# Kernel tuning notes

Measured on AMD Instinct MI355X. Metric: run time of the kernel, lower is better.

Reference implementation:

```python
import jax, jax.numpy as jnp
import numpy as np
import math

B, ENC, SEQ, H = 32, 512, 1024, 8
HD = SEQ // H  # 128
EPS = 1e-5


def setup_inputs() -> dict:
    key = jax.random.key(0)
    ks = jax.random.split(key, 7)
    s = 0.02
    return {
        "x": jax.random.normal(ks[0], (B, ENC, SEQ), jnp.float32),
        "ln_g": jnp.ones((SEQ,), jnp.float32),
        "ln_b": jnp.zeros((SEQ,), jnp.float32),
        "w_in": jax.random.normal(ks[1], (3 * SEQ, SEQ), jnp.float32) * s,
        "b_in": jnp.zeros((3 * SEQ,), jnp.float32),
        "w_m1a": jax.random.normal(ks[2], (HD, HD), jnp.float32) * s,
        "b_m1a": jnp.zeros((HD,), jnp.float32),
        "w_m1b": jax.random.normal(ks[3], (1, HD), jnp.float32) * s,
        "b_m1b": jnp.zeros((1,), jnp.float32),
        "w_m2": jax.random.normal(ks[4], (1, ENC), jnp.float32) * s,
        "b_m2": jnp.zeros((1,), jnp.float32),
        "w_out": jax.random.normal(ks[5], (SEQ, 2 * SEQ), jnp.float32) * s,
        "b_out": jnp.zeros((SEQ,), jnp.float32),
    }


def reference(x, ln_g, ln_b, w_in, b_in, w_m1a, b_m1a, w_m1b, b_m1b,
              w_m2, b_m2, w_out, b_out):
    Bsz, N, S = x.shape  # N == enc_in, S == seq_len == d_model
    hd = S // H
    scale = 1.0 / math.sqrt(hd * N)

    # LayerNorm over last dim
    mu = jnp.mean(x, axis=-1, keepdims=True)
    var = jnp.mean(jnp.square(x - mu), axis=-1, keepdims=True)
    xn = (x - mu) * jax.lax.rsqrt(var + EPS) * ln_g + ln_b

    qkv = xn @ w_in.T + b_in  # [B, N, 3S]
    q, k, v = jnp.split(qkv, 3, axis=-1)
    # torch .view(B, H, N, hd) on contiguous [B, N, S] is a raw reshape
    q = q.reshape(Bsz, H, N, hd)
    k = k.reshape(Bsz, H, N, hd)
    v = v.reshape(Bsz, H, N, hd)

    def mlp1(t):  # [B,H,N,hd] -> [B,H,N]
        h1 = jnp.maximum(jnp.einsum('bhnd,ed->bhne', t, w_m1a) + b_m1a, 0.0)
        return jnp.einsum('bhne,e->bhn', h1, w_m1b[0]) + b_m1b[0]

    def mlp2(t):  # [B,H,N,hd] -> [B,H,hd] (Linear over N then ReLU)
        return jnp.maximum(jnp.einsum('bhnd,n->bhd', t, w_m2[0]) + b_m2[0], 0.0)

    # rank-1 outer-product scores, broadcast-multiplied into v
    s_qk = mlp1(q)[..., None] * mlp2(k)[:, :, None, :] * scale  # [B,H,N,hd]
    v1 = (s_qk * v).reshape(Bsz, N, S)
    s_kq = mlp1(k)[..., None] * mlp2(q)[:, :, None, :] * scale
    v2 = (s_kq * v).reshape(Bsz, N, S)

    out = jnp.concatenate([v1, v2], axis=-1) @ w_out.T + b_out  # [B,N,S]
    return out + x  # dropout is identity at eval
```

## Files before the change

### kernel.cpp

```cpp
#include <hip/hip_runtime.h>
#include <cstdint>
#include <cstddef>

#define BSZ   32
#define ENCN  512
#define SEQL  1024
#define MROWS (BSZ*ENCN)
#define N1    (3*SEQL)
#define K1    SEQL
#define N2    SEQL
#define K2    (2*SEQL)

typedef __bf16 bf16;
typedef __bf16 bf16x8 __attribute__((ext_vector_type(8)));
typedef __bf16 bf16x4 __attribute__((ext_vector_type(4)));
typedef float  f32x4  __attribute__((ext_vector_type(4)));
typedef int    i32x4  __attribute__((ext_vector_type(4)));
typedef int    i32x8  __attribute__((ext_vector_type(8)));

__device__ __forceinline__ void gl_lds16(const void* g, void* l) {
  __builtin_amdgcn_global_load_lds(
      (const __attribute__((address_space(1))) void*)(uintptr_t)g,
      (__attribute__((address_space(3))) void*)(uintptr_t)(uint32_t)(uintptr_t)l,
      16, 0, 0);
}

__device__ __forceinline__ f32x4 mfma16(bf16x8 a, bf16x8 b, f32x4 c) {
  return __builtin_amdgcn_mfma_f32_16x16x32_bf16(a, b, c, 0, 0, 0);
}

__device__ __forceinline__ uint32_t pk4_fp8(float a, float b, float c, float d) {
  int v = __builtin_amdgcn_cvt_pk_fp8_f32(a, b, 0, false);
  v = __builtin_amdgcn_cvt_pk_fp8_f32(c, d, v, true);
  return (uint32_t)v;
}

__global__ __launch_bounds__(256) void cvt_w_kernel(const float* __restrict__ w_in,
                                                    const float* __restrict__ w_out,
                                                    const float* __restrict__ w1a,
                                                    uint8_t* __restrict__ wi8,
                                                    uint8_t* __restrict__ wo8,
                                                    bf16* __restrict__ w1ab) {
  int idx = blockIdx.x * 256 + threadIdx.x;
  const int NWIN4 = (N1 * K1) / 4;
  const int NOUT4 = (N2 * K2) / 4;
  if (idx < NWIN4) {
    float4 v = ((const float4*)w_in)[idx];
    ((uint32_t*)wi8)[idx] = pk4_fp8(v.x * 64.f, v.y * 64.f, v.z * 64.f, v.w * 64.f);
  } else if (idx < NWIN4 + NOUT4) {
    int j = idx - NWIN4;
    float4 v = ((const float4*)w_out)[j];
    ((uint32_t*)wo8)[j] = pk4_fp8(v.x * 64.f, v.y * 64.f, v.z * 64.f, v.w * 64.f);
  } else {
    int j = idx - NWIN4 - NOUT4;
    float4 v = ((const float4*)w1a)[j];
    bf16x4 o = { (bf16)v.x, (bf16)v.y, (bf16)v.z, (bf16)v.w };
    ((bf16x4*)w1ab)[j] = o;
  }
}

__global__ __launch_bounds__(256) void ln_kernel(const float* __restrict__ x,
                                                 const float* __restrict__ g,
                                                 const float* __restrict__ bt,
                                                 uint8_t* __restrict__ xn8) {
  int row = blockIdx.x;
  int t = threadIdx.x;
  const float4 v = ((const float4*)(x + (size_t)row * SEQL))[t];
  float s  = v.x + v.y + v.z + v.w;
  float ss = v.x*v.x + v.y*v.y + v.z*v.z + v.w*v.w;
  for (int off = 32; off; off >>= 1) {
    s  += __shfl_down(s,  off, 64);
    ss += __shfl_down(ss, off, 64);
  }
  __shared__ float red[8];
  int w = t >> 6, l = t & 63;
  if (l == 0) { red[w] = s; red[w + 4] = ss; }
  __syncthreads();
  float st  = red[0] + red[1] + red[2] + red[3];
  float sst = red[4] + red[5] + red[6] + red[7];
  float mu   = st * (1.0f / SEQL);
  float var  = sst * (1.0f / SEQL) - mu * mu;
  float rstd = rsqrtf(var + 1e-5f);
  float4 gv = ((const float4*)g)[t];
  float4 bv = ((const float4*)bt)[t];
  float y0 = (v.x - mu) * rstd * gv.x + bv.x;
  float y1 = (v.y - mu) * rstd * gv.y + bv.y;
  float y2 = (v.z - mu) * rstd * gv.z + bv.z;
  float y3 = (v.w - mu) * rstd * gv.w + bv.w;
  ((uint32_t*)(xn8 + (size_t)row * SEQL))[t] = pk4_fp8(y0, y1, y2, y3);
}

template <int MODE, int SA, int SB>
__global__ __launch_bounds__(256) void gemm_fp8(const uint8_t* __restrict__ A,
                                                const uint8_t* __restrict__ Bw,
                                                const float* __restrict__ bias,
                                                const float* __restrict__ resid,
                                                void* __restrict__ Cout,
                                                int M, int N, int K) {
  __shared__ uint8_t Als[128 * 128];
  __shared__ uint8_t Bls[128 * 128];
  const int tid = threadIdx.x;
  const int w = tid >> 6, l = tid & 63;
  const int wm = w & 1, wn = w >> 1;
  const int q = l >> 4, li = l & 15;
  const int m0 = blockIdx.x * 128;
  const int n0 = blockIdx.y * 128;

  const int srow = tid >> 3;
  const int scol = ((tid & 7) ^ (srow & 7)) << 4;

  const int c0 = ((2 * q)     ^ (li & 7)) << 4;
  const int c1 = ((2 * q + 1) ^ (li & 7)) << 4;

  f32x4 acc[4][4] = {};

  for (int k0 = 0; k0 < K; k0 += 128) {
#pragma unroll
    for (int is = 0; is < 4; is++) {
      gl_lds16(A  + (size_t)(m0 + is * 32 + srow) * K + k0 + scol,
               (char*)Als + is * 4096 + w * 1024);
      gl_lds16(Bw + (size_t)(n0 + is * 32 + srow) * K + k0 + scol,
               (char*)Bls + is * 4096 + w * 1024);
    }
    __syncthreads();
    i32x8 af[4], bfg[4];
#pragma unroll
    for (int i = 0; i < 4; i++) {
      int r = wm * 64 + i * 16 + li;
      i32x4 lo = *(const i32x4*)&Als[r * 128 + c0];
      i32x4 hi = *(const i32x4*)&Als[r * 128 + c1];
      af[i] = i32x8{lo[0], lo[1], lo[2], lo[3], hi[0], hi[1], hi[2], hi[3]};
    }
#pragma unroll
    for (int j = 0; j < 4; j++) {
      int r = wn * 64 + j * 16 + li;
      i32x4 lo = *(const i32x4*)&Bls[r * 128 + c0];
      i32x4 hi = *(const i32x4*)&Bls[r * 128 + c1];
      bfg[j] = i32x8{lo[0], lo[1], lo[2], lo[3], hi[0], hi[1], hi[2], hi[3]};
    }
#pragma unroll
    for (int i = 0; i < 4; i++)
#pragma unroll
      for (int j = 0; j < 4; j++)
        acc[i][j] = __builtin_amdgcn_mfma_scale_f32_16x16x128_f8f6f4(
            af[i], bfg[j], acc[i][j], 0 , 0 ,
            0, SA, 0, SB);
    __syncthreads();
  }

#pragma unroll
  for (int i = 0; i < 4; i++)
#pragma unroll
    for (int j = 0; j < 4; j++) {
      int col = n0 + wn * 64 + j * 16 + li;
      float bv = bias[col];
#pragma unroll
      for (int r = 0; r < 4; r++) {
        int row = m0 + wm * 64 + i * 16 + q * 4 + r;
        float v = acc[i][j][r] + bv;
        if (MODE == 0) {
          ((bf16*)Cout)[(size_t)row * N + col] = (bf16)v;
        } else {
          ((float*)Cout)[(size_t)row * N + col] = v + resid[(size_t)row * N + col];
        }
      }
    }
}

__global__ __launch_bounds__(256) void mlp12_kernel(const bf16* __restrict__ qkv,
                                                    const bf16* __restrict__ w1ab,
                                                    const float* __restrict__ b1a,
                                                    const float* __restrict__ w1b,
                                                    const float* __restrict__ b1b,
                                                    const float* __restrict__ w2,
                                                    float* __restrict__ A1q,
                                                    float* __restrict__ A1k,
                                                    float* __restrict__ A2p) {
  __shared__ float red1[2][128];
  __shared__ float redm[16][128];
  __shared__ float w2s[128];
  const int bid = blockIdx.x;
  const int T = bid >> 10;
  const int rem = bid & 1023;
  const int bh = rem >> 2, quarter = rem & 3;
  const int tid = threadIdx.x;
  const int w = tid >> 6, l = tid & 63;
  const int wm = w & 1, wn = w >> 1;
  const int q = l >> 4, li = l & 15;
  const int R0 = bh * 64 + quarter * 16;
  const bf16* rbase = qkv + (size_t)R0 * N1 + T * 1024;

  if (tid < 128) w2s[tid] = w2[quarter * 128 + tid];

  bf16x8 bfrag[4][4];
  float b1av[4], w1bv[4];
#pragma unroll
  for (int j = 0; j < 4; j++) {
    int n = wn * 64 + j * 16 + li;
#pragma unroll
    for (int kq = 0; kq < 4; kq++)
      bfrag[kq][j] = *(const bf16x8*)&w1ab[n * 128 + kq * 32 + q * 8];
    b1av[j] = b1a[n];
    w1bv[j] = w1b[n];
  }

  f32x4 acc[4][4] = {};
#pragma unroll
  for (int kq = 0; kq < 4; kq++) {
#pragma unroll
    for (int i = 0; i < 4; i++) {
      int lc = wm * 64 + i * 16 + li;
      bf16x8 af = *(const bf16x8*)(rbase + (size_t)(lc >> 3) * N1
                                   + (lc & 7) * 128 + kq * 32 + q * 8);
#pragma unroll
      for (int j = 0; j < 4; j++)
        acc[i][j] = mfma16(af, bfrag[kq][j], acc[i][j]);
    }
  }
#pragma unroll
  for (int i = 0; i < 4; i++)
#pragma unroll
    for (int r = 0; r < 4; r++) {
      float s = 0.f;
#pragma unroll
      for (int j = 0; j < 4; j++)
        s += fmaxf(acc[i][j][r] + b1av[j], 0.f) * w1bv[j];
      for (int off = 1; off < 16; off <<= 1) s += __shfl_xor(s, off, 64);
      if (li == 0) red1[wn][wm * 64 + i * 16 + q * 4 + r] = s;
    }
  __syncthreads();
  if (tid < 128) {
    float v = red1[0][tid] + red1[1][tid] + b1b[0];
    (T ? A1k : A1q)[bh * 512 + quarter * 128 + tid] = v;
  }

  const int rg = tid >> 4, dg = tid & 15;
  const bf16* arow = rbase + (size_t)rg * N1 + dg * 8;
  float a8[8] = {0, 0, 0, 0, 0, 0, 0, 0};
#pragma unroll
  for (int cc = 0; cc < 8; cc++) {
    bf16x8 v = *(const bf16x8*)(arow + cc * 128);
    float wgt = w2s[rg * 8 + cc];
#pragma unroll
    for (int e = 0; e < 8; e++) a8[e] += (float)v[e] * wgt;
  }
#pragma unroll
  for (int e = 0; e < 8; e++) redm[rg][dg * 8 + e] = a8[e];
  __syncthreads();
  if (tid < 128) {
    float s = 0.f;
#pragma unroll
    for (int rg2 = 0; rg2 < 16; rg2++) s += redm[rg2][tid];
    A2p[(((size_t)T * 256 + bh) * 4 + quarter) * 128 + tid] = s;
  }
}

__global__ __launch_bounds__(256) void a2c_kernel(const float* __restrict__ A2p,
                                                  const float* __restrict__ b2,
                                                  float* __restrict__ A2q,
                                                  float* __restrict__ A2k) {
  int idx = blockIdx.x * 256 + threadIdx.x;
  int t = idx >> 15, r = idx & 32767;
  int bh = r >> 7, d = r & 127;
  const float* p = A2p + ((size_t)t * 256 + bh) * 512 + d;
  float s = p[0] + p[128] + p[256] + p[384] + b2[0];
  (t ? A2k : A2q)[r] = fmaxf(s, 0.f);
}

__global__ __launch_bounds__(256) void scale_kernel(const bf16* __restrict__ qkv,
                                                    const float* __restrict__ A1q,
                                                    const float* __restrict__ A1k,
                                                    const float* __restrict__ A2q,
                                                    const float* __restrict__ A2k,
                                                    uint8_t* __restrict__ Y) {
  size_t idx = ((size_t)blockIdx.x * 256 + threadIdx.x) * 8;
  int b = (int)(idx >> 19);
  int f = (int)(idx & 524287);
  int chunk = f >> 7;
  float a1q = A1q[b * 4096 + chunk] * 64.f;
  float a1k = A1k[b * 4096 + chunk] * 64.f;
  int a2i = b * 1024 + ((f >> 16) << 7) + (f & 127);
  float4 k0 = *(const float4*)&A2k[a2i];
  float4 k1 = *(const float4*)&A2k[a2i + 4];
  float4 q0 = *(const float4*)&A2q[a2i];
  float4 q1 = *(const float4*)&A2q[a2i + 4];
  int row = b * 512 + (f >> 10);
  int col = f & 1023;
  bf16x8 v = *(const bf16x8*)&qkv[(size_t)row * N1 + 2048 + col];
  float kk[8] = { k0.x, k0.y, k0.z, k0.w, k1.x, k1.y, k1.z, k1.w };
  float qq[8] = { q0.x, q0.y, q0.z, q0.w, q1.x, q1.y, q1.z, q1.w };
  float y1[8], y2[8];
#pragma unroll
  for (int e = 0; e < 8; e++) {
    float vv = (float)v[e];
    y1[e] = a1q * kk[e] * vv;
    y2[e] = a1k * qq[e] * vv;
  }
  uint8_t* yr = Y + (size_t)row * K2;
  ((uint32_t*)(yr + col))[0] = pk4_fp8(y1[0], y1[1], y1[2], y1[3]);
  ((uint32_t*)(yr + col))[1] = pk4_fp8(y1[4], y1[5], y1[6], y1[7]);
  ((uint32_t*)(yr + 1024 + col))[0] = pk4_fp8(y2[0], y2[1], y2[2], y2[3]);
  ((uint32_t*)(yr + 1024 + col))[1] = pk4_fp8(y2[4], y2[5], y2[6], y2[7]);
}

extern "C" void kernel_launch(void* const* d_in, const int* in_sizes, int n_in,
                              void* d_out, int out_size, void* d_ws, size_t ws_size,
                              hipStream_t stream) {
  const float* x     = (const float*)d_in[0];
  const float* ln_g  = (const float*)d_in[1];
  const float* ln_b  = (const float*)d_in[2];
  const float* w_in  = (const float*)d_in[3];
  const float* b_in  = (const float*)d_in[4];
  const float* w1a   = (const float*)d_in[5];
  const float* b1a   = (const float*)d_in[6];
  const float* w1b   = (const float*)d_in[7];
  const float* b1b   = (const float*)d_in[8];
  const float* w2    = (const float*)d_in[9];
  const float* b2    = (const float*)d_in[10];
  const float* w_out = (const float*)d_in[11];
  const float* b_out = (const float*)d_in[12];
  float* out = (float*)d_out;
  char* ws = (char*)d_ws;

  uint8_t* xn8  = (uint8_t*)(ws);
  bf16*    qkv  = (bf16*)   (ws + 16777216);
  uint8_t* Y8   = (uint8_t*)(ws + 117440512);
  uint8_t* wi8  = (uint8_t*)(ws + 150994944);
  uint8_t* wo8  = (uint8_t*)(ws + 154140672);
  bf16*    w1ab = (bf16*)   (ws + 156237824);
  float*   A1q  = (float*)  (ws + 156270592);
  float*   A1k  = (float*)  (ws + 156794880);
  float*   A2p  = (float*)  (ws + 157319168);
  float*   A2q  = (float*)  (ws + 158367744);
  float*   A2k  = (float*)  (ws + 158498816);

  cvt_w_kernel<<<5136, 256, 0, stream>>>(w_in, w_out, w1a, wi8, wo8, w1ab);
  ln_kernel<<<MROWS, 256, 0, stream>>>(x, ln_g, ln_b, xn8);
  gemm_fp8<0, 127, 121><<<dim3(MROWS / 128, N1 / 128), 256, 0, stream>>>(
      xn8, wi8, b_in, nullptr, qkv, MROWS, N1, K1);
  mlp12_kernel<<<2048, 256, 0, stream>>>(qkv, w1ab, b1a, w1b, b1b, w2, A1q, A1k, A2p);
  a2c_kernel<<<256, 256, 0, stream>>>(A2p, b2, A2q, A2k);
  scale_kernel<<<8192, 256, 0, stream>>>(qkv, A1q, A1k, A2q, A2k, Y8);
  gemm_fp8<1, 113, 121><<<dim3(MROWS / 128, N2 / 128), 256, 0, stream>>>(
      Y8, wo8, b_out, x, out, MROWS, N2, K2);
}
```

Before: 324.0 us.

## Store QKV intermediate as scaled FP8 and run MLP1 with FP8 MFMA

The QKV GEMM epilogue now writes FP8 values scaled by 64 instead of bf16, halving the intermediate's size and the write and read traffic in the MLP and scale kernels. MLP1 switches to FP8 MFMA with FP8 weights, and the scale factors are folded into the downstream kernels. The workspace layout is compacted and Y8 reuses the LN buffer region. The risk is lower precision in q/k/v, which feeds the rank-1 score products.

```diff
diff --git a/kernel.cpp b/kernel.cpp
--- a/kernel.cpp
+++ b/kernel.cpp
@@ -1,4 +1,5 @@
 #include <hip/hip_runtime.h>
+#include <hip/hip_fp8.h>
 #include <cstdint>
 #include <cstddef>
 
@@ -12,8 +13,6 @@
 #define K2    (2*SEQL)
 
 typedef __bf16 bf16;
-typedef __bf16 bf16x8 __attribute__((ext_vector_type(8)));
-typedef __bf16 bf16x4 __attribute__((ext_vector_type(4)));
 typedef float  f32x4  __attribute__((ext_vector_type(4)));
 typedef int    i32x4  __attribute__((ext_vector_type(4)));
 typedef int    i32x8  __attribute__((ext_vector_type(8)));
@@ -25,14 +24,20 @@
       16, 0, 0);
 }
 
-__device__ __forceinline__ f32x4 mfma16(bf16x8 a, bf16x8 b, f32x4 c) {
-  return __builtin_amdgcn_mfma_f32_16x16x32_bf16(a, b, c, 0, 0, 0);
-}
-
 __device__ __forceinline__ uint32_t pk4_fp8(float a, float b, float c, float d) {
   int v = __builtin_amdgcn_cvt_pk_fp8_f32(a, b, 0, false);
   v = __builtin_amdgcn_cvt_pk_fp8_f32(c, d, v, true);
   return (uint32_t)v;
+}
+__device__ __forceinline__ uint8_t pk1_fp8(float a) {
+  return (uint8_t)(__builtin_amdgcn_cvt_pk_fp8_f32(a, a, 0, false) & 0xff);
+}
+__device__ __forceinline__ float fp8_to_f(uint32_t b) {
+  __hip_fp8_e4m3 t; t.__x = (__hip_fp8_storage_t)b; return (float)t;
+}
+
+__device__ __forceinline__ f32x4 mfma8(long a, long b, f32x4 c) {
+  return __builtin_amdgcn_mfma_f32_16x16x32_fp8_fp8(a, b, c, 0, 0, 0);
 }
 
 __global__ __launch_bounds__(256) void cvt_w_kernel(const float* __restrict__ w_in,
@@ -40,23 +45,22 @@
                                                     const float* __restrict__ w1a,
                                                     uint8_t* __restrict__ wi8,
                                                     uint8_t* __restrict__ wo8,
-                                                    bf16* __restrict__ w1ab) {
+                                                    uint8_t* __restrict__ w1a8) {
   int idx = blockIdx.x * 256 + threadIdx.x;
   const int NWIN4 = (N1 * K1) / 4;
   const int NOUT4 = (N2 * K2) / 4;
+  const float4* src;
+  uint32_t* dst;
+  int j;
   if (idx < NWIN4) {
-    float4 v = ((const float4*)w_in)[idx];
-    ((uint32_t*)wi8)[idx] = pk4_fp8(v.x * 64.f, v.y * 64.f, v.z * 64.f, v.w * 64.f);
+    src = (const float4*)w_in;  dst = (uint32_t*)wi8;  j = idx;
   } else if (idx < NWIN4 + NOUT4) {
-    int j = idx - NWIN4;
-    float4 v = ((const float4*)w_out)[j];
-    ((uint32_t*)wo8)[j] = pk4_fp8(v.x * 64.f, v.y * 64.f, v.z * 64.f, v.w * 64.f);
+    src = (const float4*)w_out; dst = (uint32_t*)wo8;  j = idx - NWIN4;
   } else {
-    int j = idx - NWIN4 - NOUT4;
-    float4 v = ((const float4*)w1a)[j];
-    bf16x4 o = { (bf16)v.x, (bf16)v.y, (bf16)v.z, (bf16)v.w };
-    ((bf16x4*)w1ab)[j] = o;
-  }
+    src = (const float4*)w1a;   dst = (uint32_t*)w1a8; j = idx - NWIN4 - NOUT4;
+  }
+  float4 v = src[j];
+  dst[j] = pk4_fp8(v.x * 64.f, v.y * 64.f, v.z * 64.f, v.w * 64.f);
 }
 
 __global__ __launch_bounds__(256) void ln_kernel(const float* __restrict__ x,
@@ -91,12 +95,12 @@
 }
 
 template <int MODE, int SA, int SB>
-__global__ __launch_bounds__(256) void gemm_fp8(const uint8_t* __restrict__ A,
-                                                const uint8_t* __restrict__ Bw,
-                                                const float* __restrict__ bias,
-                                                const float* __restrict__ resid,
-                                                void* __restrict__ Cout,
-                                                int M, int N, int K) {
+__device__ __forceinline__ void gemm_fp8_impl(const uint8_t* __restrict__ A,
+                                              const uint8_t* __restrict__ Bw,
+                                              const float* __restrict__ bias,
+                                              const float* __restrict__ resid,
+                                              void* __restrict__ Cout,
+                                              int M, int N, int K) {
   __shared__ uint8_t Als[128 * 128];
   __shared__ uint8_t Bls[128 * 128];
   const int tid = threadIdx.x;
@@ -159,7 +163,7 @@
         int row = m0 + wm * 64 + i * 16 + q * 4 + r;
         float v = acc[i][j][r] + bv;
         if (MODE == 0) {
-          ((bf16*)Cout)[(size_t)row * N + col] = (bf16)v;
+          ((uint8_t*)Cout)[(size_t)row * N + col] = pk1_fp8(v * 64.f);
         } else {
           ((float*)Cout)[(size_t)row * N + col] = v + resid[(size_t)row * N + col];
         }
@@ -167,8 +171,22 @@
     }
 }
 
-__global__ __launch_bounds__(256) void mlp12_kernel(const bf16* __restrict__ qkv,
-                                                    const bf16* __restrict__ w1ab,
+__global__ __launch_bounds__(256) void gemm_qkv(const uint8_t* __restrict__ A,
+                                                const uint8_t* __restrict__ Bw,
+                                                const float* __restrict__ bias,
+                                                uint8_t* __restrict__ Cout) {
+  gemm_fp8_impl<0, 127, 121>(A, Bw, bias, nullptr, Cout, MROWS, N1, K1);
+}
+__global__ __launch_bounds__(256) void gemm_out(const uint8_t* __restrict__ A,
+                                                const uint8_t* __restrict__ Bw,
+                                                const float* __restrict__ bias,
+                                                const float* __restrict__ resid,
+                                                float* __restrict__ Cout) {
+  gemm_fp8_impl<1, 113, 121>(A, Bw, bias, resid, Cout, MROWS, N2, K2);
+}
+
+__global__ __launch_bounds__(256) void mlp12_kernel(const uint8_t* __restrict__ qkv8,
+                                                    const uint8_t* __restrict__ w1a8,
                                                     const float* __restrict__ b1a,
                                                     const float* __restrict__ w1b,
                                                     const float* __restrict__ b1b,
@@ -188,18 +206,18 @@
   const int wm = w & 1, wn = w >> 1;
   const int q = l >> 4, li = l & 15;
   const int R0 = bh * 64 + quarter * 16;
-  const bf16* rbase = qkv + (size_t)R0 * N1 + T * 1024;
+  const uint8_t* rbase = qkv8 + (size_t)R0 * N1 + T * 1024;
 
   if (tid < 128) w2s[tid] = w2[quarter * 128 + tid];
 
-  bf16x8 bfrag[4][4];
+  long bfrag[4][4];
   float b1av[4], w1bv[4];
 #pragma unroll
   for (int j = 0; j < 4; j++) {
     int n = wn * 64 + j * 16 + li;
 #pragma unroll
     for (int kq = 0; kq < 4; kq++)
-      bfrag[kq][j] = *(const bf16x8*)&w1ab[n * 128 + kq * 32 + q * 8];
+      bfrag[kq][j] = *(const long*)&w1a8[n * 128 + kq * 32 + q * 8];
     b1av[j] = b1a[n];
     w1bv[j] = w1b[n];
   }
@@ -210,13 +228,14 @@
 #pragma unroll
     for (int i = 0; i < 4; i++) {
       int lc = wm * 64 + i * 16 + li;
-      bf16x8 af = *(const bf16x8*)(rbase + (size_t)(lc >> 3) * N1
-                                   + (lc & 7) * 128 + kq * 32 + q * 8);
+      long af = *(const long*)(rbase + (size_t)(lc >> 3) * N1
+                               + (lc & 7) * 128 + kq * 32 + q * 8);
 #pragma unroll
       for (int j = 0; j < 4; j++)
-        acc[i][j] = mfma16(af, bfrag[kq][j], acc[i][j]);
-    }
-  }
+        acc[i][j] = mfma8(af, bfrag[kq][j], acc[i][j]);
+    }
+  }
+  const float inv4096 = 1.0f / 4096.0f;
 #pragma unroll
   for (int i = 0; i < 4; i++)
 #pragma unroll
@@ -224,7 +243,7 @@
       float s = 0.f;
 #pragma unroll
       for (int j = 0; j < 4; j++)
-        s += fmaxf(acc[i][j][r] + b1av[j], 0.f) * w1bv[j];
+        s += fmaxf(acc[i][j][r] * inv4096 + b1av[j], 0.f) * w1bv[j];
       for (int off = 1; off < 16; off <<= 1) s += __shfl_xor(s, off, 64);
       if (li == 0) red1[wn][wm * 64 + i * 16 + q * 4 + r] = s;
     }
@@ -235,14 +254,15 @@
   }
 
   const int rg = tid >> 4, dg = tid & 15;
-  const bf16* arow = rbase + (size_t)rg * N1 + dg * 8;
+  const uint8_t* arow = rbase + (size_t)rg * N1 + dg * 8;
   float a8[8] = {0, 0, 0, 0, 0, 0, 0, 0};
 #pragma unroll
   for (int cc = 0; cc < 8; cc++) {
-    bf16x8 v = *(const bf16x8*)(arow + cc * 128);
+    uint64_t vb = *(const uint64_t*)(arow + cc * 128);
     float wgt = w2s[rg * 8 + cc];
 #pragma unroll
-    for (int e = 0; e < 8; e++) a8[e] += (float)v[e] * wgt;
+    for (int e = 0; e < 8; e++)
+      a8[e] += fp8_to_f((uint32_t)(vb >> (8 * e)) & 0xff) * wgt;
   }
 #pragma unroll
   for (int e = 0; e < 8; e++) redm[rg][dg * 8 + e] = a8[e];
@@ -263,11 +283,11 @@
   int t = idx >> 15, r = idx & 32767;
   int bh = r >> 7, d = r & 127;
   const float* p = A2p + ((size_t)t * 256 + bh) * 512 + d;
-  float s = p[0] + p[128] + p[256] + p[384] + b2[0];
+  float s = (p[0] + p[128] + p[256] + p[384]) * (1.0f / 64.0f) + b2[0];
   (t ? A2k : A2q)[r] = fmaxf(s, 0.f);
 }
 
-__global__ __launch_bounds__(256) void scale_kernel(const bf16* __restrict__ qkv,
+__global__ __launch_bounds__(256) void scale_kernel(const uint8_t* __restrict__ qkv8,
                                                     const float* __restrict__ A1q,
                                                     const float* __restrict__ A1k,
                                                     const float* __restrict__ A2q,
@@ -277,8 +297,8 @@
   int b = (int)(idx >> 19);
   int f = (int)(idx & 524287);
   int chunk = f >> 7;
-  float a1q = A1q[b * 4096 + chunk] * 64.f;
-  float a1k = A1k[b * 4096 + chunk] * 64.f;
+  float a1q = A1q[b * 4096 + chunk];
+  float a1k = A1k[b * 4096 + chunk];
   int a2i = b * 1024 + ((f >> 16) << 7) + (f & 127);
   float4 k0 = *(const float4*)&A2k[a2i];
   float4 k1 = *(const float4*)&A2k[a2i + 4];
@@ -286,15 +306,15 @@
   float4 q1 = *(const float4*)&A2q[a2i + 4];
   int row = b * 512 + (f >> 10);
   int col = f & 1023;
-  bf16x8 v = *(const bf16x8*)&qkv[(size_t)row * N1 + 2048 + col];
+  uint64_t vb = *(const uint64_t*)(qkv8 + (size_t)row * N1 + 2048 + col);
   float kk[8] = { k0.x, k0.y, k0.z, k0.w, k1.x, k1.y, k1.z, k1.w };
   float qq[8] = { q0.x, q0.y, q0.z, q0.w, q1.x, q1.y, q1.z, q1.w };
   float y1[8], y2[8];
 #pragma unroll
   for (int e = 0; e < 8; e++) {
-    float vv = (float)v[e];
-    y1[e] = a1q * kk[e] * vv;
-    y2[e] = a1k * qq[e] * vv;
+    float v64 = fp8_to_f((uint32_t)(vb >> (8 * e)) & 0xff);
+    y1[e] = a1q * kk[e] * v64;
+    y2[e] = a1k * qq[e] * v64;
   }
   uint8_t* yr = Y + (size_t)row * K2;
   ((uint32_t*)(yr + col))[0] = pk4_fp8(y1[0], y1[1], y1[2], y1[3]);
@@ -323,24 +343,22 @@
   char* ws = (char*)d_ws;
 
   uint8_t* xn8  = (uint8_t*)(ws);
-  bf16*    qkv  = (bf16*)   (ws + 16777216);
-  uint8_t* Y8   = (uint8_t*)(ws + 117440512);
-  uint8_t* wi8  = (uint8_t*)(ws + 150994944);
-  uint8_t* wo8  = (uint8_t*)(ws + 154140672);
-  bf16*    w1ab = (bf16*)   (ws + 156237824);
-  float*   A1q  = (float*)  (ws + 156270592);
-  float*   A1k  = (float*)  (ws + 156794880);
-  float*   A2p  = (float*)  (ws + 157319168);
-  float*   A2q  = (float*)  (ws + 158367744);
-  float*   A2k  = (float*)  (ws + 158498816);
-
-  cvt_w_kernel<<<5136, 256, 0, stream>>>(w_in, w_out, w1a, wi8, wo8, w1ab);
+  uint8_t* Y8   = (uint8_t*)(ws);
+  uint8_t* qkv8 = (uint8_t*)(ws + 33554432);
+  uint8_t* wi8  = (uint8_t*)(ws + 83886080);
+  uint8_t* wo8  = (uint8_t*)(ws + 87031808);
+  uint8_t* w1a8 = (uint8_t*)(ws + 89128960);
+  float*   A1q  = (float*)  (ws + 89145344);
+  float*   A1k  = (float*)  (ws + 89669632);
+  float*   A2p  = (float*)  (ws + 90193920);
+  float*   A2q  = (float*)  (ws + 91242496);
+  float*   A2k  = (float*)  (ws + 91373568);
+
+  cvt_w_kernel<<<5136, 256, 0, stream>>>(w_in, w_out, w1a, wi8, wo8, w1a8);
   ln_kernel<<<MROWS, 256, 0, stream>>>(x, ln_g, ln_b, xn8);
-  gemm_fp8<0, 127, 121><<<dim3(MROWS / 128, N1 / 128), 256, 0, stream>>>(
-      xn8, wi8, b_in, nullptr, qkv, MROWS, N1, K1);
-  mlp12_kernel<<<2048, 256, 0, stream>>>(qkv, w1ab, b1a, w1b, b1b, w2, A1q, A1k, A2p);
+  gemm_qkv<<<dim3(MROWS / 128, N1 / 128), 256, 0, stream>>>(xn8, wi8, b_in, qkv8);
+  mlp12_kernel<<<2048, 256, 0, stream>>>(qkv8, w1a8, b1a, w1b, b1b, w2, A1q, A1k, A2p);
   a2c_kernel<<<256, 256, 0, stream>>>(A2p, b2, A2q, A2k);
-  scale_kernel<<<8192, 256, 0, stream>>>(qkv, A1q, A1k, A2q, A2k, Y8);
-  gemm_fp8<1, 113, 121><<<dim3(MROWS / 128, N2 / 128), 256, 0, stream>>>(
-      Y8, wo8, b_out, x, out, MROWS, N2, K2);
-}
+  scale_kernel<<<8192, 256, 0, stream>>>(qkv8, A1q, A1k, A2q, A2k, Y8);
+  gemm_out<<<dim3(MROWS / 128, N2 / 128), 256, 0, stream>>>(Y8, wo8, b_out, x, out);
+}
```

After: 325.9 us. About the same (+0.6%).
